# Kernel tuning notes

Hardware: AMD Instinct MI355X
Metric: run time of the kernel (lower is better)

## Reference

```python
import jax, jax.numpy as jnp
import numpy as np

N_SEQ, SEQ_LEN, BATCH, IN, H, OUT = 32, 256, 16, 32, 256, 1


def setup_inputs() -> dict:
    key = jax.random.key(0)
    ks = jax.random.split(key, 12)
    s = 1.0 / np.sqrt(H)  # torch RNNCell default init scale
    f32 = jnp.float32
    return {
        "x": jax.random.normal(ks[0], (N_SEQ, SEQ_LEN, BATCH, IN), f32),
        "flags": jax.random.randint(ks[1], (N_SEQ,), 0, 2, dtype=jnp.int32),
        "W_ih1": jax.random.normal(ks[2], (2, 4 * H, IN), f32) * s,
        "W_hh1": jax.random.normal(ks[3], (2, 4 * H, H), f32) * s,
        "b_ih1": jax.random.normal(ks[4], (2, 4 * H), f32) * s,
        "b_hh1": jax.random.normal(ks[5], (2, 4 * H), f32) * s,
        "W_ih2": jax.random.normal(ks[6], (4 * H, H), f32) * s,
        "W_hh2": jax.random.normal(ks[7], (4 * H, H), f32) * s,
        "b_ih2": jax.random.normal(ks[8], (4 * H,), f32) * s,
        "b_hh2": jax.random.normal(ks[9], (4 * H,), f32) * s,
        "W_lin": jax.random.normal(ks[10], (OUT, H), f32) * s,
        "b_lin": jax.random.normal(ks[11], (OUT,), f32) * s,
    }


def _lstm_cell(xt, h, c, Wih, Whh, b):
    # torch LSTMCell: gates = x@Wih.T + h@Whh.T + b_ih + b_hh; chunks i,f,g,o
    gates = xt @ Wih.T + h @ Whh.T + b
    i, f, g, o = jnp.split(gates, 4, axis=-1)
    c = jax.nn.sigmoid(f) * c + jax.nn.sigmoid(i) * jnp.tanh(g)
    h = jax.nn.sigmoid(o) * jnp.tanh(c)
    return h, c


def reference(x, flags, W_ih1, W_hh1, b_ih1, b_hh1,
              W_ih2, W_hh2, b_ih2, b_hh2, W_lin, b_lin):
    # flags selects layer1 (on-paper, idx 0) vs layer1_air (idx 1) per sequence
    Wih_s = W_ih1[flags]              # [N_SEQ, 4H, IN]
    Whh_s = W_hh1[flags]              # [N_SEQ, 4H, H]
    b_s = (b_ih1 + b_hh1)[flags]      # [N_SEQ, 4H]

    h0 = jnp.zeros((BATCH, H), x.dtype)

    def run_seq(xs, Wih, Whh, b):
        # hidden resets to zero at the start of every sequence -> independent scans
        def step(carry, xt):
            h, c = _lstm_cell(xt, *carry, Wih, Whh, b)
            return (h, c), None
        (h, _), _ = jax.lax.scan(step, (h0, h0), xs)
        return h

    h1 = jax.vmap(run_seq)(x, Wih_s, Whh_s, b_s)  # [N_SEQ, BATCH, H]

    # layer2: sequential LSTM over per-sequence final hiddens (dropout=0 -> identity)
    b2 = b_ih2 + b_hh2

    def step2(carry, hin):
        h, c = _lstm_cell(hin, *carry, W_ih2, W_hh2, b2)
        return (h, c), None

    (h2, _), _ = jax.lax.scan(step2, (h0, h0), h1)
    return jax.nn.sigmoid(h2 @ W_lin.T + b_lin)  # [BATCH, OUT]
```

## Files before the change

### kernel.cpp

```cpp
#include <hip/hip_runtime.h>
#include <hip/hip_bf16.h>

#define NSEQ   32
#define SEQLEN 256
#define NB     16
#define NIN    32
#define NH     256
#define G4     1024

#define PROBE_T 2

typedef __attribute__((ext_vector_type(8))) short bf16x8;
typedef __attribute__((ext_vector_type(4))) float f32x4;
typedef unsigned long long ull;

__device__ __forceinline__ unsigned short f2bf(float f) {
    union { float f; unsigned u; } v; v.f = f;
    unsigned u = v.u;
    return (unsigned short)((u + 0x7FFFu + ((u >> 16) & 1u)) >> 16);
}
__device__ __forceinline__ float bf2f(unsigned short u) {
    union { unsigned u; float f; } v; v.u = ((unsigned)u) << 16; return v.f;
}
__device__ __forceinline__ float sigf(float x) { return 1.0f / (1.0f + __expf(-x)); }
__device__ __forceinline__ float tanhfast(float x) { return 1.0f - 2.0f / (__expf(2.0f * x) + 1.0f); }

__global__ void pack_w1(const float* __restrict__ Wih, const float* __restrict__ Whh,
                        unsigned short* __restrict__ Bp) {
    int idx = blockIdx.x * blockDim.x + threadIdx.x;
    if (idx >= 2 * 64 * 9 * 64) return;
    int fl   = idx / (64 * 9 * 64);
    int rem  = idx % (64 * 9 * 64);
    int tile = rem / (9 * 64);
    int kk   = (rem / 64) % 9;
    int l    = rem & 63;
    int n    = tile * 16 + (l & 15);
    int k0   = kk * 32 + (l >> 4) * 8;
    unsigned short* dst = Bp + (size_t)idx * 8;
#pragma unroll
    for (int j = 0; j < 8; ++j) {
        int k = k0 + j;
        float v = (k < NH) ? Whh[((size_t)fl * G4 + n) * NH + k]
                           : Wih[((size_t)fl * G4 + n) * NIN + (k - NH)];
        dst[j] = f2bf(v);
    }
}

__global__ void pack_w2(const float* __restrict__ Wih, const float* __restrict__ Whh,
                        unsigned short* __restrict__ Bp) {
    int idx = blockIdx.x * blockDim.x + threadIdx.x;
    if (idx >= 64 * 16 * 64) return;
    int tile = idx / (16 * 64);
    int kk   = (idx / 64) % 16;
    int l    = idx & 63;
    int n    = tile * 16 + (l & 15);
    int k0   = kk * 32 + (l >> 4) * 8;
    unsigned short* dst = Bp + (size_t)idx * 8;
#pragma unroll
    for (int j = 0; j < 8; ++j) {
        int k = k0 + j;
        float v = (k < NH) ? Whh[(size_t)n * NH + k] : Wih[(size_t)n * NH + (k - NH)];
        dst[j] = f2bf(v);
    }
}

#define STRA 320
#define ASH_BYTES (NB * STRA * 2)

__device__ __forceinline__ unsigned aoff(int row, int col) {
    return (((unsigned)(row * STRA + col)) * 2u) ^ (((unsigned)row & 7u) << 4);
}

__global__ __launch_bounds__(1024) void lstm_layer1(
    const float* __restrict__ x, const int* __restrict__ flags,
    const float* __restrict__ bih, const float* __restrict__ bhh,
    const unsigned short* __restrict__ Bp_all,
    unsigned short* __restrict__ h1bf,
    unsigned* __restrict__ hxS,
    unsigned* __restrict__ hxF,
    unsigned* __restrict__ vslot)
{
    __shared__ __align__(16) unsigned char Ash[ASH_BYTES];
    __shared__ float gate[4][64][17];
    __shared__ int s_fail, s_groupF;

    const int bid = blockIdx.x;
    const int s   = bid & 31;
    const int j   = bid >> 5;
    const int tid = threadIdx.x;
    const int w = tid >> 6, l = tid & 63, lr = l & 15, kg = l >> 4;
    const int g = w >> 2, cg = w & 3;
    const int fl = flags[s];
    const int tile = g * 16 + j * 4 + cg;
    const unsigned short* Bp = Bp_all + (size_t)fl * (64 * 9 * 64 * 8);

    bf16x8 wreg[9];
#pragma unroll
    for (int kk = 0; kk < 9; ++kk)
        wreg[kk] = *(const bf16x8*)(Bp + ((size_t)(tile * 9 + kk) * 64 + l) * 8);

    const int grow = tile * 16 + lr;
    const float bias = bih[fl * G4 + grow] + bhh[fl * G4 + grow];

    const int pb = tid >> 6, pc = tid & 63;
    const int o0 = (((j + 1) & 3) << 6) + pc;
    const int o1 = (((j + 2) & 3) << 6) + pc;
    const int o2 = (((j + 3) & 3) << 6) + pc;
    const int xb = tid >> 5, xk = tid & 31;
    float cst = 0.f;
    int mode = 0;
    bool groupF = false;

    unsigned* hxSs = hxS + (size_t)s * (2 * NB * 256);
    unsigned* hxFs = hxF + (size_t)s * (2 * NB * 256);

    if (tid == 0) { s_fail = 0; s_groupF = 0; }
    for (int i = tid * 4; i < ASH_BYTES; i += 1024 * 4)
        *(unsigned*)(Ash + i) = 0u;
    __syncthreads();
    if (tid < NB * NIN)
        *(unsigned short*)(Ash + aoff(xb, NH + xk)) =
            f2bf(x[(((size_t)s * SEQLEN) * NB + xb) * NIN + xk]);
    __syncthreads();

    for (int t = 0; t < SEQLEN; ++t) {
        float xpre = 0.f;
        if (t + 1 < SEQLEN && tid < NB * NIN)
            xpre = x[(((size_t)s * SEQLEN + t + 1) * NB + xb) * NIN + xk];

        f32x4 acc = {bias, bias, bias, bias};
        f32x4 accB = {0.f, 0.f, 0.f, 0.f};
#pragma unroll
        for (int kk = 0; kk < 5; ++kk) {
            bf16x8 a = *(const bf16x8*)(Ash + aoff(lr, kk * 32 + kg * 8));
            acc = __builtin_amdgcn_mfma_f32_16x16x32_bf16(a, wreg[kk], acc, 0, 0, 0);
        }
#pragma unroll
        for (int kk = 5; kk < 9; ++kk) {
            bf16x8 a = *(const bf16x8*)(Ash + aoff(lr, kk * 32 + kg * 8));
            accB = __builtin_amdgcn_mfma_f32_16x16x32_bf16(a, wreg[kk], accB, 0, 0, 0);
        }
#pragma unroll
        for (int r = 0; r < 4; ++r)
            gate[g][cg * 16 + lr][kg * 4 + r] = acc[r] + accB[r];
        __syncthreads();

        float ig = gate[0][pc][pb], fg = gate[1][pc][pb];
        float gg = gate[2][pc][pb], og = gate[3][pc][pb];
        float cn = sigf(fg) * cst + sigf(ig) * tanhfast(gg);
        cst = cn;
        float h = sigf(og) * tanhfast(cn);
        unsigned short hb = f2bf(h);
        *(unsigned short*)(Ash + aoff(pb, (j << 6) + pc)) = hb;

        if (t == SEQLEN - 1) {
            h1bf[((size_t)s * NB + pb) * NH + (j << 6) + pc] = hb;
        } else {
            const unsigned tg = (unsigned)(t + 1);
            const unsigned word = ((unsigned)hb << 16) | tg;
            const size_t ro = (size_t)((((t + 1) & 1) * NB + pb) << 8);
            unsigned* rowF = hxFs + ro;
            unsigned* rowS = hxSs + ro;
            volatile const unsigned* F = rowF;

            rowF[(j << 6) + pc] = word;
            const bool pubS = (t < PROBE_T) || !groupF;
            if (pubS)
                __hip_atomic_store(rowS + (j << 6) + pc, word,
                                   __ATOMIC_RELAXED, __HIP_MEMORY_SCOPE_AGENT);
            unsigned v0 = F[o0], v1 = F[o1], v2 = F[o2];
            if (tid < NB * NIN)
                *(unsigned short*)(Ash + aoff(xb, NH + xk)) = f2bf(xpre);

            if (groupF) {
                while ((v0 & 0xFFFFu) != tg) v0 = F[o0];
                while ((v1 & 0xFFFFu) != tg) v1 = F[o1];
                while ((v2 & 0xFFFFu) != tg) v2 = F[o2];
            } else {
                bool ok = false;
                if (mode != 2) {
                    int budget = (mode == 0) ? 300 : 4000;
                    while ((v0 & 0xFFFFu) != tg && budget-- > 0) v0 = F[o0];
                    while ((v1 & 0xFFFFu) != tg && budget-- > 0) v1 = F[o1];
                    while ((v2 & 0xFFFFu) != tg && budget-- > 0) v2 = F[o2];
                    ok = ((v0 & 0xFFFFu) == tg) && ((v1 & 0xFFFFu) == tg) && ((v2 & 0xFFFFu) == tg);
                    if (t >= PROBE_T) mode = ok ? 1 : 2;
                }
                if (!ok) {
                    if (t < PROBE_T) s_fail = 1;
                    v0 = __hip_atomic_load(rowS + o0, __ATOMIC_RELAXED, __HIP_MEMORY_SCOPE_AGENT);
                    v1 = __hip_atomic_load(rowS + o1, __ATOMIC_RELAXED, __HIP_MEMORY_SCOPE_AGENT);
                    v2 = __hip_atomic_load(rowS + o2, __ATOMIC_RELAXED, __HIP_MEMORY_SCOPE_AGENT);
                    while ((v0 & 0xFFFFu) != tg)
                        v0 = __hip_atomic_load(rowS + o0, __ATOMIC_RELAXED, __HIP_MEMORY_SCOPE_AGENT);
                    while ((v1 & 0xFFFFu) != tg)
                        v1 = __hip_atomic_load(rowS + o1, __ATOMIC_RELAXED, __HIP_MEMORY_SCOPE_AGENT);
                    while ((v2 & 0xFFFFu) != tg)
                        v2 = __hip_atomic_load(rowS + o2, __ATOMIC_RELAXED, __HIP_MEMORY_SCOPE_AGENT);
                }
            }
            *(unsigned short*)(Ash + aoff(pb, o0)) = (unsigned short)(v0 >> 16);
            *(unsigned short*)(Ash + aoff(pb, o1)) = (unsigned short)(v1 >> 16);
            *(unsigned short*)(Ash + aoff(pb, o2)) = (unsigned short)(v2 >> 16);
            __syncthreads();

            if (t == PROBE_T - 1) {
                if (tid == 0) {
                    unsigned verdict = (s_fail == 0) ? 2u : 1u;
                    __hip_atomic_store(vslot + s * 4 + j, verdict,
                                       __ATOMIC_RELAXED, __HIP_MEMORY_SCOPE_AGENT);
                    unsigned a0, a1, a2, a3;
                    do {
                        a0 = __hip_atomic_load(vslot + s * 4 + 0, __ATOMIC_RELAXED, __HIP_MEMORY_SCOPE_AGENT);
                        a1 = __hip_atomic_load(vslot + s * 4 + 1, __ATOMIC_RELAXED, __HIP_MEMORY_SCOPE_AGENT);
                        a2 = __hip_atomic_load(vslot + s * 4 + 2, __ATOMIC_RELAXED, __HIP_MEMORY_SCOPE_AGENT);
                        a3 = __hip_atomic_load(vslot + s * 4 + 3, __ATOMIC_RELAXED, __HIP_MEMORY_SCOPE_AGENT);
                    } while (!(a0 && a1 && a2 && a3));
                    s_groupF = (a0 == 2u && a1 == 2u && a2 == 2u && a3 == 2u) ? 1 : 0;
                }
                __syncthreads();
                groupF = (s_groupF != 0);
            }
        }
    }
}

#define STRA2 520

__global__ __launch_bounds__(1024) void lstm_layer2(
    const unsigned short* __restrict__ h1bf,
    const float* __restrict__ bih2, const float* __restrict__ bhh2,
    const unsigned short* __restrict__ Bp2,
    const float* __restrict__ Wlin, const float* __restrict__ blin,
    float* __restrict__ out,
    unsigned* __restrict__ hx2S,
    unsigned* __restrict__ hx2F,
    unsigned* __restrict__ vslot2)
{
    const int bid = blockIdx.x;
    if (bid & 7) return;
    const int j = bid >> 3;

    __shared__ __align__(16) unsigned short A_sh[NB * STRA2];
    __shared__ float gate[4][64][17];
    __shared__ float red[NB * 16];
    __shared__ int s_fail, s_groupF;

    const int tid = threadIdx.x;
    const int w = tid >> 6, l = tid & 63, lr = l & 15, kg = l >> 4;
    const int g = w >> 2, cg = w & 3;
    const int tile = g * 16 + j * 4 + cg;

    bf16x8 wreg[16];
#pragma unroll
    for (int kk = 0; kk < 16; ++kk)
        wreg[kk] = *(const bf16x8*)(Bp2 + ((size_t)(tile * 16 + kk) * 64 + l) * 8);

    const int grow = tile * 16 + lr;
    const float bias = bih2[grow] + bhh2[grow];
    const int pb = tid >> 6, pc = tid & 63;
    float cst = 0.f;
    int mode = 0;
    bool groupF = false;
    const int rb = tid >> 6, rc4 = (tid & 63) * 4;
    const int q0 = (((j + 1) & 3) << 6) + pc;
    const int q1 = (((j + 2) & 3) << 6) + pc;
    const int q2 = (((j + 3) & 3) << 6) + pc;

    if (tid == 0) { s_fail = 0; s_groupF = 0; }
    for (int i = tid; i < NB * NH; i += 1024)
        A_sh[(i >> 8) * STRA2 + (i & 255)] = 0;
    *(ushort4*)&A_sh[rb * STRA2 + NH + rc4] = *(const ushort4*)&h1bf[(size_t)rb * NH + rc4];
    __syncthreads();

    for (int sq = 0; sq < NSEQ; ++sq) {
        ushort4 pre = {0, 0, 0, 0};
        if (sq + 1 < NSEQ)
            pre = *(const ushort4*)&h1bf[((size_t)(sq + 1) * NB + rb) * NH + rc4];

        f32x4 acc = {bias, bias, bias, bias};
        f32x4 accB = {0.f, 0.f, 0.f, 0.f};
#pragma unroll
        for (int kk = 0; kk < 8; ++kk) {
            bf16x8 a = *(const bf16x8*)&A_sh[lr * STRA2 + kk * 32 + kg * 8];
            acc = __builtin_amdgcn_mfma_f32_16x16x32_bf16(a, wreg[kk], acc, 0, 0, 0);
        }
#pragma unroll
        for (int kk = 8; kk < 16; ++kk) {
            bf16x8 a = *(const bf16x8*)&A_sh[lr * STRA2 + kk * 32 + kg * 8];
            accB = __builtin_amdgcn_mfma_f32_16x16x32_bf16(a, wreg[kk], accB, 0, 0, 0);
        }
#pragma unroll
        for (int r = 0; r < 4; ++r)
            gate[g][cg * 16 + lr][kg * 4 + r] = acc[r] + accB[r];
        __syncthreads();

        const unsigned tg = (unsigned)(sq + 1);
        const size_t ro = (size_t)((((sq + 1) & 1) * NB + pb) << 8);
        unsigned* rowF = hx2F + ro;
        unsigned* rowS = hx2S + ro;
        volatile const unsigned* F = rowF;
        {
            float ig = gate[0][pc][pb], fg = gate[1][pc][pb];
            float gg = gate[2][pc][pb], og = gate[3][pc][pb];
            float cn = sigf(fg) * cst + sigf(ig) * tanhfast(gg);
            cst = cn;
            float h = sigf(og) * tanhfast(cn);
            unsigned word = ((unsigned)f2bf(h) << 16) | tg;
            A_sh[pb * STRA2 + (j << 6) + pc] = (unsigned short)(word >> 16);
            rowF[(j << 6) + pc] = word;
            if ((sq < PROBE_T) || !groupF)
                __hip_atomic_store(rowS + (j << 6) + pc, word,
                                   __ATOMIC_RELAXED, __HIP_MEMORY_SCOPE_AGENT);
        }
        unsigned v0 = F[q0], v1 = F[q1], v2 = F[q2];
        if (sq + 1 < NSEQ)
            *(ushort4*)&A_sh[rb * STRA2 + NH + rc4] = pre;

        if (groupF) {
            while ((v0 & 0xFFFFu) != tg) v0 = F[q0];
            while ((v1 & 0xFFFFu) != tg) v1 = F[q1];
            while ((v2 & 0xFFFFu) != tg) v2 = F[q2];
        } else {
            bool ok = false;
            if (mode != 2) {
                int budget = (mode == 0) ? 300 : 4000;
                while ((v0 & 0xFFFFu) != tg && budget-- > 0) v0 = F[q0];
                while ((v1 & 0xFFFFu) != tg && budget-- > 0) v1 = F[q1];
                while ((v2 & 0xFFFFu) != tg && budget-- > 0) v2 = F[q2];
                ok = ((v0 & 0xFFFFu) == tg) && ((v1 & 0xFFFFu) == tg) && ((v2 & 0xFFFFu) == tg);
                if (sq >= PROBE_T) mode = ok ? 1 : 2;
            }
            if (!ok) {
                if (sq < PROBE_T) s_fail = 1;
                v0 = __hip_atomic_load(rowS + q0, __ATOMIC_RELAXED, __HIP_MEMORY_SCOPE_AGENT);
                v1 = __hip_atomic_load(rowS + q1, __ATOMIC_RELAXED, __HIP_MEMORY_SCOPE_AGENT);
                v2 = __hip_atomic_load(rowS + q2, __ATOMIC_RELAXED, __HIP_MEMORY_SCOPE_AGENT);
                while ((v0 & 0xFFFFu) != tg)
                    v0 = __hip_atomic_load(rowS + q0, __ATOMIC_RELAXED, __HIP_MEMORY_SCOPE_AGENT);
                while ((v1 & 0xFFFFu) != tg)
                    v1 = __hip_atomic_load(rowS + q1, __ATOMIC_RELAXED, __HIP_MEMORY_SCOPE_AGENT);
                while ((v2 & 0xFFFFu) != tg)
                    v2 = __hip_atomic_load(rowS + q2, __ATOMIC_RELAXED, __HIP_MEMORY_SCOPE_AGENT);
            }
        }
        A_sh[pb * STRA2 + q0] = (unsigned short)(v0 >> 16);
        A_sh[pb * STRA2 + q1] = (unsigned short)(v1 >> 16);
        A_sh[pb * STRA2 + q2] = (unsigned short)(v2 >> 16);
        __syncthreads();

        if (sq == PROBE_T - 1) {
            if (tid == 0) {
                unsigned verdict = (s_fail == 0) ? 2u : 1u;
                __hip_atomic_store(vslot2 + j, verdict, __ATOMIC_RELAXED, __HIP_MEMORY_SCOPE_AGENT);
                unsigned a0, a1, a2, a3;
                do {
                    a0 = __hip_atomic_load(vslot2 + 0, __ATOMIC_RELAXED, __HIP_MEMORY_SCOPE_AGENT);
                    a1 = __hip_atomic_load(vslot2 + 1, __ATOMIC_RELAXED, __HIP_MEMORY_SCOPE_AGENT);
                    a2 = __hip_atomic_load(vslot2 + 2, __ATOMIC_RELAXED, __HIP_MEMORY_SCOPE_AGENT);
                    a3 = __hip_atomic_load(vslot2 + 3, __ATOMIC_RELAXED, __HIP_MEMORY_SCOPE_AGENT);
                } while (!(a0 && a1 && a2 && a3));
                s_groupF = (a0 == 2u && a1 == 2u && a2 == 2u && a3 == 2u) ? 1 : 0;
            }
            __syncthreads();
            groupF = (s_groupF != 0);
        }
    }

    if (j == 0) {
        if (tid < 256) {
            int b = tid >> 4, kc = tid & 15;
            float pacc = 0.f;
#pragma unroll
            for (int k = 0; k < 16; ++k)
                pacc += bf2f(A_sh[b * STRA2 + kc * 16 + k]) * Wlin[kc * 16 + k];
            red[b * 16 + kc] = pacc;
        }
        __syncthreads();
        if (tid < 16) {
            float ssum = blin[0];
#pragma unroll
            for (int kc = 0; kc < 16; ++kc) ssum += red[tid * 16 + kc];
            out[tid] = 1.0f / (1.0f + __expf(-ssum));
        }
    }
}

extern "C" void kernel_launch(void* const* d_in, const int* in_sizes, int n_in,
                              void* d_out, int out_size, void* d_ws, size_t ws_size,
                              hipStream_t stream) {
    const float* x    = (const float*)d_in[0];
    const int*   flg  = (const int*)d_in[1];
    const float* Wih1 = (const float*)d_in[2];
    const float* Whh1 = (const float*)d_in[3];
    const float* bih1 = (const float*)d_in[4];
    const float* bhh1 = (const float*)d_in[5];
    const float* Wih2 = (const float*)d_in[6];
    const float* Whh2 = (const float*)d_in[7];
    const float* bih2 = (const float*)d_in[8];
    const float* bhh2 = (const float*)d_in[9];
    const float* Wlin = (const float*)d_in[10];
    const float* blin = (const float*)d_in[11];
    float* out = (float*)d_out;

    unsigned short* ws   = (unsigned short*)d_ws;
    unsigned short* Bp1  = ws;
    unsigned short* Bp2  = Bp1 + 589824;
    unsigned short* h1bf = Bp2 + 524288;
    unsigned*       hxS1 = (unsigned*)(h1bf + 131072);
    unsigned*       hxF1 = hxS1 + 262144;
    unsigned*       hx2S = hxF1 + 262144;
    unsigned*       hx2F = hx2S + 8192;
    unsigned*       vs1  = hx2F + 8192;
    unsigned*       vs2  = vs1 + 128;

    hipMemsetAsync(hxS1, 0, (size_t)(262144 * 2 + 8192 * 2 + 132) * 4, stream);

    pack_w1<<<dim3(288), dim3(256), 0, stream>>>(Wih1, Whh1, Bp1);
    pack_w2<<<dim3(256), dim3(256), 0, stream>>>(Wih2, Whh2, Bp2);
    lstm_layer1<<<dim3(128), dim3(1024), 0, stream>>>(x, flg, bih1, bhh1, Bp1, h1bf,
                                                      hxS1, hxF1, vs1);
    lstm_layer2<<<dim3(32), dim3(1024), 0, stream>>>(h1bf, bih2, bhh2, Bp2, Wlin, blin, out,
                                                     hx2S, hx2F, vs2);
}
```

Before: 575.3 us.

## Split layer-1 LSTM across two blocks per sequence with register-resident gates

Layer 1 now uses 64 blocks of 512 threads, two per sequence, instead of 128 blocks of 1024 threads, four per sequence. Each wave computes all four gates (i, f, g, o) for its 16 hidden columns, so the cell update happens in registers without the shared gate buffer and its block barrier. The A operand is double-buffered in LDS so one barrier per step suffices. Cross-block exchange now reads 128 columns from a single peer block instead of three, which halves the handshake group. The cost is four times the weight registers per thread (36 bf16x8 fragments) and twice the serial MFMA chain per wave.

```diff
diff --git a/kernel.cpp b/kernel.cpp
--- a/kernel.cpp
+++ b/kernel.cpp
@@ -71,7 +71,7 @@
     return (((unsigned)(row * STRA + col)) * 2u) ^ (((unsigned)row & 7u) << 4);
 }
 
-__global__ __launch_bounds__(1024) void lstm_layer1(
+__global__ __launch_bounds__(512, 2) void lstm_layer1(
     const float* __restrict__ x, const int* __restrict__ flags,
     const float* __restrict__ bih, const float* __restrict__ bhh,
     const unsigned short* __restrict__ Bp_all,
@@ -80,8 +80,7 @@
     unsigned* __restrict__ hxF,
     unsigned* __restrict__ vslot)
 {
-    __shared__ __align__(16) unsigned char Ash[ASH_BYTES];
-    __shared__ float gate[4][64][17];
+    __shared__ __align__(16) unsigned char Ash[2][ASH_BYTES];
     __shared__ int s_fail, s_groupF;
 
     const int bid = blockIdx.x;
@@ -89,25 +88,28 @@
     const int j   = bid >> 5;
     const int tid = threadIdx.x;
     const int w = tid >> 6, l = tid & 63, lr = l & 15, kg = l >> 4;
-    const int g = w >> 2, cg = w & 3;
+    const int ct = j * 8 + w;
+    const int m  = ct * 16 + lr;
     const int fl = flags[s];
-    const int tile = g * 16 + j * 4 + cg;
     const unsigned short* Bp = Bp_all + (size_t)fl * (64 * 9 * 64 * 8);
 
-    bf16x8 wreg[9];
-#pragma unroll
-    for (int kk = 0; kk < 9; ++kk)
-        wreg[kk] = *(const bf16x8*)(Bp + ((size_t)(tile * 9 + kk) * 64 + l) * 8);
-
-    const int grow = tile * 16 + lr;
-    const float bias = bih[fl * G4 + grow] + bhh[fl * G4 + grow];
-
-    const int pb = tid >> 6, pc = tid & 63;
-    const int o0 = (((j + 1) & 3) << 6) + pc;
-    const int o1 = (((j + 2) & 3) << 6) + pc;
-    const int o2 = (((j + 3) & 3) << 6) + pc;
-    const int xb = tid >> 5, xk = tid & 31;
-    float cst = 0.f;
+    bf16x8 wreg[4][9];
+#pragma unroll
+    for (int g = 0; g < 4; ++g)
+#pragma unroll
+        for (int kk = 0; kk < 9; ++kk)
+            wreg[g][kk] = *(const bf16x8*)(Bp + ((size_t)((g * 16 + ct) * 9 + kk) * 64 + l) * 8);
+
+    float bias[4];
+#pragma unroll
+    for (int g = 0; g < 4; ++g)
+        bias[g] = bih[fl * G4 + (g * 16 + ct) * 16 + lr] + bhh[fl * G4 + (g * 16 + ct) * 16 + lr];
+
+    float cst[4] = {0.f, 0.f, 0.f, 0.f};
+
+    const int rb  = tid >> 5;
+    const int rc0 = ((1 - j) << 7) + (tid & 31) * 4;
+    const int xb  = tid >> 5, xk = tid & 31;
     int mode = 0;
     bool groupF = false;
 
@@ -115,93 +117,101 @@
     unsigned* hxFs = hxF + (size_t)s * (2 * NB * 256);
 
     if (tid == 0) { s_fail = 0; s_groupF = 0; }
-    for (int i = tid * 4; i < ASH_BYTES; i += 1024 * 4)
-        *(unsigned*)(Ash + i) = 0u;
+    for (int i = tid * 4; i < 2 * ASH_BYTES; i += 512 * 4)
+        *(unsigned*)(&Ash[0][0] + i) = 0u;
     __syncthreads();
-    if (tid < NB * NIN)
-        *(unsigned short*)(Ash + aoff(xb, NH + xk)) =
-            f2bf(x[(((size_t)s * SEQLEN) * NB + xb) * NIN + xk]);
+    *(unsigned short*)(&Ash[0][0] + aoff(xb, NH + xk)) =
+        f2bf(x[(((size_t)s * SEQLEN) * NB + xb) * NIN + xk]);
     __syncthreads();
 
     for (int t = 0; t < SEQLEN; ++t) {
+        const int cur = t & 1, nxt = cur ^ 1;
         float xpre = 0.f;
-        if (t + 1 < SEQLEN && tid < NB * NIN)
+        if (t + 1 < SEQLEN)
             xpre = x[(((size_t)s * SEQLEN + t + 1) * NB + xb) * NIN + xk];
 
-        f32x4 acc = {bias, bias, bias, bias};
-        f32x4 accB = {0.f, 0.f, 0.f, 0.f};
-#pragma unroll
-        for (int kk = 0; kk < 5; ++kk) {
-            bf16x8 a = *(const bf16x8*)(Ash + aoff(lr, kk * 32 + kg * 8));
-            acc = __builtin_amdgcn_mfma_f32_16x16x32_bf16(a, wreg[kk], acc, 0, 0, 0);
-        }
-#pragma unroll
-        for (int kk = 5; kk < 9; ++kk) {
-            bf16x8 a = *(const bf16x8*)(Ash + aoff(lr, kk * 32 + kg * 8));
-            accB = __builtin_amdgcn_mfma_f32_16x16x32_bf16(a, wreg[kk], accB, 0, 0, 0);
-        }
-#pragma unroll
-        for (int r = 0; r < 4; ++r)
-            gate[g][cg * 16 + lr][kg * 4 + r] = acc[r] + accB[r];
-        __syncthreads();
-
-        float ig = gate[0][pc][pb], fg = gate[1][pc][pb];
-        float gg = gate[2][pc][pb], og = gate[3][pc][pb];
-        float cn = sigf(fg) * cst + sigf(ig) * tanhfast(gg);
-        cst = cn;
-        float h = sigf(og) * tanhfast(cn);
-        unsigned short hb = f2bf(h);
-        *(unsigned short*)(Ash + aoff(pb, (j << 6) + pc)) = hb;
+        f32x4 acc0 = {bias[0], bias[0], bias[0], bias[0]};
+        f32x4 acc1 = {bias[1], bias[1], bias[1], bias[1]};
+        f32x4 acc2 = {bias[2], bias[2], bias[2], bias[2]};
+        f32x4 acc3 = {bias[3], bias[3], bias[3], bias[3]};
+#pragma unroll
+        for (int kk = 0; kk < 9; ++kk) {
+            bf16x8 a = *(const bf16x8*)(Ash[cur] + aoff(lr, kk * 32 + kg * 8));
+            acc0 = __builtin_amdgcn_mfma_f32_16x16x32_bf16(a, wreg[0][kk], acc0, 0, 0, 0);
+            acc1 = __builtin_amdgcn_mfma_f32_16x16x32_bf16(a, wreg[1][kk], acc1, 0, 0, 0);
+            acc2 = __builtin_amdgcn_mfma_f32_16x16x32_bf16(a, wreg[2][kk], acc2, 0, 0, 0);
+            acc3 = __builtin_amdgcn_mfma_f32_16x16x32_bf16(a, wreg[3][kk], acc3, 0, 0, 0);
+        }
+
+        unsigned short hb[4];
+#pragma unroll
+        for (int r = 0; r < 4; ++r) {
+            float cn = sigf(acc1[r]) * cst[r] + sigf(acc0[r]) * tanhfast(acc2[r]);
+            cst[r] = cn;
+            hb[r] = f2bf(sigf(acc3[r]) * tanhfast(cn));
+        }
 
         if (t == SEQLEN - 1) {
-            h1bf[((size_t)s * NB + pb) * NH + (j << 6) + pc] = hb;
+#pragma unroll
+            for (int r = 0; r < 4; ++r)
+                h1bf[((size_t)s * NB + (kg * 4 + r)) * NH + m] = hb[r];
         } else {
             const unsigned tg = (unsigned)(t + 1);
-            const unsigned word = ((unsigned)hb << 16) | tg;
-            const size_t ro = (size_t)((((t + 1) & 1) * NB + pb) << 8);
-            unsigned* rowF = hxFs + ro;
-            unsigned* rowS = hxSs + ro;
+            unsigned* rowF = hxFs + (nxt * NB * 256);
+            unsigned* rowS = hxSs + (nxt * NB * 256);
             volatile const unsigned* F = rowF;
 
-            rowF[(j << 6) + pc] = word;
+#pragma unroll
+            for (int r = 0; r < 4; ++r) {
+                const int b = kg * 4 + r;
+                *(unsigned short*)(Ash[nxt] + aoff(b, m)) = hb[r];
+                rowF[b * 256 + m] = ((unsigned)hb[r] << 16) | tg;
+            }
             const bool pubS = (t < PROBE_T) || !groupF;
-            if (pubS)
-                __hip_atomic_store(rowS + (j << 6) + pc, word,
-                                   __ATOMIC_RELAXED, __HIP_MEMORY_SCOPE_AGENT);
-            unsigned v0 = F[o0], v1 = F[o1], v2 = F[o2];
-            if (tid < NB * NIN)
-                *(unsigned short*)(Ash + aoff(xb, NH + xk)) = f2bf(xpre);
+            if (pubS) {
+#pragma unroll
+                for (int r = 0; r < 4; ++r) {
+                    const int b = kg * 4 + r;
+                    __hip_atomic_store(rowS + b * 256 + m, ((unsigned)hb[r] << 16) | tg,
+                                       __ATOMIC_RELAXED, __HIP_MEMORY_SCOPE_AGENT);
+                }
+            }
+            unsigned v0 = F[rb * 256 + rc0 + 0];
+            unsigned v1 = F[rb * 256 + rc0 + 1];
+            unsigned v2 = F[rb * 256 + rc0 + 2];
+            unsigned v3 = F[rb * 256 + rc0 + 3];
+            *(unsigned short*)(Ash[nxt] + aoff(xb, NH + xk)) = f2bf(xpre);
 
             if (groupF) {
-                while ((v0 & 0xFFFFu) != tg) v0 = F[o0];
-                while ((v1 & 0xFFFFu) != tg) v1 = F[o1];
-                while ((v2 & 0xFFFFu) != tg) v2 = F[o2];
+                while ((v0 & 0xFFFFu) != tg) v0 = F[rb * 256 + rc0 + 0];
+                while ((v1 & 0xFFFFu) != tg) v1 = F[rb * 256 + rc0 + 1];
+                while ((v2 & 0xFFFFu) != tg) v2 = F[rb * 256 + rc0 + 2];
+                while ((v3 & 0xFFFFu) != tg) v3 = F[rb * 256 + rc0 + 3];
             } else {
                 bool ok = false;
                 if (mode != 2) {
                     int budget = (mode == 0) ? 300 : 4000;
-                    while ((v0 & 0xFFFFu) != tg && budget-- > 0) v0 = F[o0];
-                    while ((v1 & 0xFFFFu) != tg && budget-- > 0) v1 = F[o1];
-                    while ((v2 & 0xFFFFu) != tg && budget-- > 0) v2 = F[o2];
-                    ok = ((v0 & 0xFFFFu) == tg) && ((v1 & 0xFFFFu) == tg) && ((v2 & 0xFFFFu) == tg);
+                    while ((v0 & 0xFFFFu) != tg && budget-- > 0) v0 = F[rb * 256 + rc0 + 0];
+                    while ((v1 & 0xFFFFu) != tg && budget-- > 0) v1 = F[rb * 256 + rc0 + 1];
+                    while ((v2 & 0xFFFFu) != tg && budget-- > 0) v2 = F[rb * 256 + rc0 + 2];
+                    while ((v3 & 0xFFFFu) != tg && budget-- > 0) v3 = F[rb * 256 + rc0 + 3];
+                    ok = ((v0 & 0xFFFFu) == tg) && ((v1 & 0xFFFFu) == tg) &&
+                         ((v2 & 0xFFFFu) == tg) && ((v3 & 0xFFFFu) == tg);
                     if (t >= PROBE_T) mode = ok ? 1 : 2;
                 }
                 if (!ok) {
                     if (t < PROBE_T) s_fail = 1;
-                    v0 = __hip_atomic_load(rowS + o0, __ATOMIC_RELAXED, __HIP_MEMORY_SCOPE_AGENT);
-                    v1 = __hip_atomic_load(rowS + o1, __ATOMIC_RELAXED, __HIP_MEMORY_SCOPE_AGENT);
-                    v2 = __hip_atomic_load(rowS + o2, __ATOMIC_RELAXED, __HIP_MEMORY_SCOPE_AGENT);
-                    while ((v0 & 0xFFFFu) != tg)
-                        v0 = __hip_atomic_load(rowS + o0, __ATOMIC_RELAXED, __HIP_MEMORY_SCOPE_AGENT);
-                    while ((v1 & 0xFFFFu) != tg)
-                        v1 = __hip_atomic_load(rowS + o1, __ATOMIC_RELAXED, __HIP_MEMORY_SCOPE_AGENT);
-                    while ((v2 & 0xFFFFu) != tg)
-                        v2 = __hip_atomic_load(rowS + o2, __ATOMIC_RELAXED, __HIP_MEMORY_SCOPE_AGENT);
+                    const unsigned* Srow = rowS + rb * 256 + rc0;
+                    do { v0 = __hip_atomic_load(Srow + 0, __ATOMIC_RELAXED, __HIP_MEMORY_SCOPE_AGENT); } while ((v0 & 0xFFFFu) != tg);
+                    do { v1 = __hip_atomic_load(Srow + 1, __ATOMIC_RELAXED, __HIP_MEMORY_SCOPE_AGENT); } while ((v1 & 0xFFFFu) != tg);
+                    do { v2 = __hip_atomic_load(Srow + 2, __ATOMIC_RELAXED, __HIP_MEMORY_SCOPE_AGENT); } while ((v2 & 0xFFFFu) != tg);
+                    do { v3 = __hip_atomic_load(Srow + 3, __ATOMIC_RELAXED, __HIP_MEMORY_SCOPE_AGENT); } while ((v3 & 0xFFFFu) != tg);
                 }
             }
-            *(unsigned short*)(Ash + aoff(pb, o0)) = (unsigned short)(v0 >> 16);
-            *(unsigned short*)(Ash + aoff(pb, o1)) = (unsigned short)(v1 >> 16);
-            *(unsigned short*)(Ash + aoff(pb, o2)) = (unsigned short)(v2 >> 16);
+            ushort4 pv;
+            pv.x = (unsigned short)(v0 >> 16); pv.y = (unsigned short)(v1 >> 16);
+            pv.z = (unsigned short)(v2 >> 16); pv.w = (unsigned short)(v3 >> 16);
+            *(ushort4*)(Ash[nxt] + aoff(rb, rc0)) = pv;
             __syncthreads();
 
             if (t == PROBE_T - 1) {
@@ -209,14 +219,12 @@
                     unsigned verdict = (s_fail == 0) ? 2u : 1u;
                     __hip_atomic_store(vslot + s * 4 + j, verdict,
                                        __ATOMIC_RELAXED, __HIP_MEMORY_SCOPE_AGENT);
-                    unsigned a0, a1, a2, a3;
+                    unsigned a0, a1;
                     do {
                         a0 = __hip_atomic_load(vslot + s * 4 + 0, __ATOMIC_RELAXED, __HIP_MEMORY_SCOPE_AGENT);
                         a1 = __hip_atomic_load(vslot + s * 4 + 1, __ATOMIC_RELAXED, __HIP_MEMORY_SCOPE_AGENT);
-                        a2 = __hip_atomic_load(vslot + s * 4 + 2, __ATOMIC_RELAXED, __HIP_MEMORY_SCOPE_AGENT);
-                        a3 = __hip_atomic_load(vslot + s * 4 + 3, __ATOMIC_RELAXED, __HIP_MEMORY_SCOPE_AGENT);
-                    } while (!(a0 && a1 && a2 && a3));
-                    s_groupF = (a0 == 2u && a1 == 2u && a2 == 2u && a3 == 2u) ? 1 : 0;
+                    } while (!(a0 && a1));
+                    s_groupF = (a0 == 2u && a1 == 2u) ? 1 : 0;
                 }
                 __syncthreads();
                 groupF = (s_groupF != 0);
@@ -333,15 +341,9 @@
             }
             if (!ok) {
                 if (sq < PROBE_T) s_fail = 1;
-                v0 = __hip_atomic_load(rowS + q0, __ATOMIC_RELAXED, __HIP_MEMORY_SCOPE_AGENT);
-                v1 = __hip_atomic_load(rowS + q1, __ATOMIC_RELAXED, __HIP_MEMORY_SCOPE_AGENT);
-                v2 = __hip_atomic_load(rowS + q2, __ATOMIC_RELAXED, __HIP_MEMORY_SCOPE_AGENT);
-                while ((v0 & 0xFFFFu) != tg)
-                    v0 = __hip_atomic_load(rowS + q0, __ATOMIC_RELAXED, __HIP_MEMORY_SCOPE_AGENT);
-                while ((v1 & 0xFFFFu) != tg)
-                    v1 = __hip_atomic_load(rowS + q1, __ATOMIC_RELAXED, __HIP_MEMORY_SCOPE_AGENT);
-                while ((v2 & 0xFFFFu) != tg)
-                    v2 = __hip_atomic_load(rowS + q2, __ATOMIC_RELAXED, __HIP_MEMORY_SCOPE_AGENT);
+                do { v0 = __hip_atomic_load(rowS + q0, __ATOMIC_RELAXED, __HIP_MEMORY_SCOPE_AGENT); } while ((v0 & 0xFFFFu) != tg);
+                do { v1 = __hip_atomic_load(rowS + q1, __ATOMIC_RELAXED, __HIP_MEMORY_SCOPE_AGENT); } while ((v1 & 0xFFFFu) != tg);
+                do { v2 = __hip_atomic_load(rowS + q2, __ATOMIC_RELAXED, __HIP_MEMORY_SCOPE_AGENT); } while ((v2 & 0xFFFFu) != tg);
             }
         }
         A_sh[pb * STRA2 + q0] = (unsigned short)(v0 >> 16);
@@ -418,8 +420,8 @@
 
     pack_w1<<<dim3(288), dim3(256), 0, stream>>>(Wih1, Whh1, Bp1);
     pack_w2<<<dim3(256), dim3(256), 0, stream>>>(Wih2, Whh2, Bp2);
-    lstm_layer1<<<dim3(128), dim3(1024), 0, stream>>>(x, flg, bih1, bhh1, Bp1, h1bf,
-                                                      hxS1, hxF1, vs1);
+    lstm_layer1<<<dim3(64), dim3(512), 0, stream>>>(x, flg, bih1, bhh1, Bp1, h1bf,
+                                                    hxS1, hxF1, vs1);
     lstm_layer2<<<dim3(32), dim3(1024), 0, stream>>>(h1bf, bih2, bhh2, Bp2, Wlin, blin, out,
                                                      hx2S, hx2F, vs2);
 }
```

After: 759.6 us. +32.0%, slower.
